# Performance work log

Hardware: AMD Instinct MI355X
Metric: run time of the kernel (lower is better)

Reference implementation:

```python
import jax, jax.numpy as jnp
import numpy as np

T = 4096          # tokens (batch*seq)
D = 768           # moe_intermediate_size (token hidden dim)
I = 2048          # intermediate_size (FFN inner dim)
E = 8             # num_experts


def setup_inputs() -> dict:
    key = jax.random.key(0)
    k_x, k_p, k_g, k_u, k_d = jax.random.split(key, 5)
    hidden_states = jax.random.normal(k_x, (T, D), dtype=jnp.float32)
    position_index = jax.random.randint(k_p, (T,), 0, E, dtype=jnp.int64)
    behavior_index = jnp.zeros((T,), dtype=jnp.int64)  # unused (behavior_injection=False)
    s = 0.02
    # torch Linear weight layout: [out_features, in_features]
    gate_w = jax.random.normal(k_g, (E, I, D), dtype=jnp.float32) * s
    up_w = jax.random.normal(k_u, (E, I, D), dtype=jnp.float32) * s
    down_w = jax.random.normal(k_d, (E, D, I), dtype=jnp.float32) * s
    return {
        "hidden_states": hidden_states,
        "position_index": position_index,
        "behavior_index": behavior_index,
        "gate_w": gate_w,
        "up_w": up_w,
        "down_w": down_w,
    }


def reference(hidden_states, position_index, behavior_index, gate_w, up_w, down_w):
    # Sparse MoE dispatch: each token routed to exactly one expert by position_index.
    # Dropout rate is 0.0 (eval) -> identity. behavior_injection=False -> behavior_index unused.
    num_experts = gate_w.shape[0]
    out = jnp.zeros_like(hidden_states)
    for e in range(num_experts):  # structural loop over fixed expert count
        mask = (position_index == e)[:, None]          # [T, 1]
        g = hidden_states @ gate_w[e].T                 # [T, I]
        u = hidden_states @ up_w[e].T                   # [T, I]
        y = (jax.nn.silu(g) * u) @ down_w[e].T          # [T, D]
        out = out + jnp.where(mask, y, 0.0)             # scatter-combine
    return out
```

## Files before the change

### kernel.cpp

```cpp
#include <hip/hip_runtime.h>
#include <hip/hip_bf16.h>

#define T_TOK 4096
#define DDIM  768
#define IDIM  2048
#define NEXP  8

typedef __attribute__((ext_vector_type(8))) short  bfrag;
typedef __attribute__((ext_vector_type(4))) float  ffrag;

static __device__ __forceinline__ unsigned short f2bf(float f) {
    union { float f; unsigned u; } v; v.f = f;
    unsigned r = v.u + 0x7FFFu + ((v.u >> 16) & 1u);
    return (unsigned short)(r >> 16);
}

static __device__ __forceinline__ unsigned cvt2(float x, float y) {
    return (unsigned)f2bf(x) | ((unsigned)f2bf(y) << 16);
}

__global__ void k_sort(const int* __restrict__ pos, int* __restrict__ ws_i,
                       int* __restrict__ perm) {
    __shared__ int hist[NEXP], cursor[NEXP];
    const int tid = threadIdx.x;
    if (tid < NEXP) hist[tid] = 0;
    __syncthreads();
    for (int i = tid; i < T_TOK; i += 1024)
        atomicAdd(&hist[pos[i]], 1);
    __syncthreads();
    if (tid == 0) {
        int s = 0;
        for (int e = 0; e < NEXP; ++e) {
            cursor[e] = s;
            ws_i[e] = hist[e];
            ws_i[16 + e] = s;
            s += hist[e];
        }
        ws_i[16 + NEXP] = s;
    }
    __syncthreads();
    for (int i = tid; i < T_TOK; i += 1024) {
        int p = atomicAdd(&cursor[pos[i]], 1);
        perm[p] = i;
    }
}

__global__ void k_gather(const float* __restrict__ x, const int* __restrict__ perm,
                         unsigned short* __restrict__ xg) {
    int p = blockIdx.x;
    int tok = perm[p];
    int j = threadIdx.x * 4;
    const float4 v = *reinterpret_cast<const float4*>(x + (size_t)tok * DDIM + j);
    uint2 o;
    o.x = cvt2(v.x, v.y);
    o.y = cvt2(v.z, v.w);
    *reinterpret_cast<uint2*>(xg + (size_t)p * DDIM + j) = o;
}

__launch_bounds__(256, 2)
__global__ void k_gemm1(const unsigned short* __restrict__ xg,
                        const float* __restrict__ gate_w,
                        const float* __restrict__ up_w,
                        unsigned short* __restrict__ hg,
                        const int* __restrict__ ws_i) {
    const int e   = blockIdx.z;
    const int cnt = ws_i[e];
    const int m0  = blockIdx.y * 128;
    if (m0 >= cnt) return;
    const int off = ws_i[16 + e];
    const int n0  = blockIdx.x * 64;

    const int tid  = threadIdx.x;
    const int lane = tid & 63;
    const int wave = tid >> 6;
    const int wm   = wave & 1;
    const int wn   = wave >> 1;

    __shared__ __align__(16) unsigned short lsA[128 * 56];
    __shared__ __align__(16) unsigned short lsG[64 * 56];
    __shared__ __align__(16) unsigned short lsU[64 * 56];

    const float* gate_e = gate_w + (size_t)e * (IDIM * DDIM);
    const float* up_e   = up_w   + (size_t)e * (IDIM * DDIM);

    const int ar = tid >> 2;
    const int aq = tid & 3;
    const int br = tid >> 3;
    const int bq = tid & 7;

    int g0 = off + m0 + ar;      if (g0 > T_TOK - 1) g0 = T_TOK - 1;
    int g1 = off + m0 + ar + 64; if (g1 > T_TOK - 1) g1 = T_TOK - 1;
    const unsigned short* a0p = xg + (size_t)g0 * DDIM + aq * 8;
    const unsigned short* a1p = xg + (size_t)g1 * DDIM + aq * 8;
    const float* gp0 = gate_e + (size_t)(n0 + br)      * DDIM + bq * 4;
    const float* gp1 = gate_e + (size_t)(n0 + br + 32) * DDIM + bq * 4;
    const float* up0 = up_e   + (size_t)(n0 + br)      * DDIM + bq * 4;
    const float* up1 = up_e   + (size_t)(n0 + br + 32) * DDIM + bq * 4;

    uint4  pa0 = *reinterpret_cast<const uint4*>(a0p);
    uint4  pa1 = *reinterpret_cast<const uint4*>(a1p);
    float4 pg0 = *reinterpret_cast<const float4*>(gp0);
    float4 pg1 = *reinterpret_cast<const float4*>(gp1);
    float4 pu0 = *reinterpret_cast<const float4*>(up0);
    float4 pu1 = *reinterpret_cast<const float4*>(up1);

    ffrag accG[4][2], accU[4][2];
    const ffrag fz = {0.f, 0.f, 0.f, 0.f};
    for (int mi = 0; mi < 4; ++mi)
        for (int ni = 0; ni < 2; ++ni) { accG[mi][ni] = fz; accU[mi][ni] = fz; }

    const int koff = (lane >> 4) * 8;
    const int rsel = lane & 15;

    for (int kt = 0; kt < DDIM / 32; ++kt) {
        *reinterpret_cast<uint4*>(&lsA[ar * 56 + aq * 8])        = pa0;
        *reinterpret_cast<uint4*>(&lsA[(ar + 64) * 56 + aq * 8]) = pa1;
        { uint2 o; o.x = cvt2(pg0.x, pg0.y); o.y = cvt2(pg0.z, pg0.w);
          *reinterpret_cast<uint2*>(&lsG[br * 56 + bq * 4]) = o; }
        { uint2 o; o.x = cvt2(pg1.x, pg1.y); o.y = cvt2(pg1.z, pg1.w);
          *reinterpret_cast<uint2*>(&lsG[(br + 32) * 56 + bq * 4]) = o; }
        { uint2 o; o.x = cvt2(pu0.x, pu0.y); o.y = cvt2(pu0.z, pu0.w);
          *reinterpret_cast<uint2*>(&lsU[br * 56 + bq * 4]) = o; }
        { uint2 o; o.x = cvt2(pu1.x, pu1.y); o.y = cvt2(pu1.z, pu1.w);
          *reinterpret_cast<uint2*>(&lsU[(br + 32) * 56 + bq * 4]) = o; }
        __syncthreads();

        if (kt < DDIM / 32 - 1) {
            const int kb = (kt + 1) * 32;
            pa0 = *reinterpret_cast<const uint4*>(a0p + kb);
            pa1 = *reinterpret_cast<const uint4*>(a1p + kb);
            pg0 = *reinterpret_cast<const float4*>(gp0 + kb);
            pg1 = *reinterpret_cast<const float4*>(gp1 + kb);
            pu0 = *reinterpret_cast<const float4*>(up0 + kb);
            pu1 = *reinterpret_cast<const float4*>(up1 + kb);
        }

        bfrag a[4], bg[2], bu[2];
        #pragma unroll
        for (int mi = 0; mi < 4; ++mi)
            a[mi] = *reinterpret_cast<const bfrag*>(&lsA[(wm * 64 + mi * 16 + rsel) * 56 + koff]);
        #pragma unroll
        for (int ni = 0; ni < 2; ++ni) {
            bg[ni] = *reinterpret_cast<const bfrag*>(&lsG[(wn * 32 + ni * 16 + rsel) * 56 + koff]);
            bu[ni] = *reinterpret_cast<const bfrag*>(&lsU[(wn * 32 + ni * 16 + rsel) * 56 + koff]);
        }
        #pragma unroll
        for (int mi = 0; mi < 4; ++mi)
            #pragma unroll
            for (int ni = 0; ni < 2; ++ni) {
                accG[mi][ni] = __builtin_amdgcn_mfma_f32_16x16x32_bf16(a[mi], bg[ni], accG[mi][ni], 0, 0, 0);
                accU[mi][ni] = __builtin_amdgcn_mfma_f32_16x16x32_bf16(a[mi], bu[ni], accU[mi][ni], 0, 0, 0);
            }
        __syncthreads();
    }

    const int colb  = lane & 15;
    const int rquad = (lane >> 4) * 4;
    #pragma unroll
    for (int mi = 0; mi < 4; ++mi)
        #pragma unroll
        for (int ni = 0; ni < 2; ++ni) {
            int n = n0 + wn * 32 + ni * 16 + colb;
            #pragma unroll
            for (int r = 0; r < 4; ++r) {
                int ml = wm * 64 + mi * 16 + rquad + r;
                if (m0 + ml < cnt) {
                    float g = accG[mi][ni][r];
                    float u = accU[mi][ni][r];
                    float h = (g / (1.0f + __expf(-g))) * u;
                    hg[(size_t)(off + m0 + ml) * IDIM + n] = f2bf(h);
                }
            }
        }
}

__launch_bounds__(256, 2)
__global__ void k_gemm2(const unsigned short* __restrict__ hg,
                        const float* __restrict__ down_w,
                        float* __restrict__ out,
                        const int* __restrict__ ws_i,
                        const int* __restrict__ perm) {
    const int e     = blockIdx.z & 7;
    const int split = blockIdx.z >> 3;
    const int cnt = ws_i[e];
    const int m0  = blockIdx.y * 128;
    if (m0 >= cnt) return;
    const int off = ws_i[16 + e];
    const int n0  = blockIdx.x * 64;

    const int tid  = threadIdx.x;
    const int lane = tid & 63;
    const int wave = tid >> 6;
    const int wm   = wave & 1;
    const int wn   = wave >> 1;

    __shared__ __align__(16) unsigned short lsA[128 * 56];
    __shared__ __align__(16) unsigned short lsB[64 * 56];

    const float* down_e = down_w + (size_t)e * (DDIM * IDIM);

    const int ar = tid >> 2;
    const int aq = tid & 3;
    const int br = tid >> 3;
    const int bq = tid & 7;

    int g0 = off + m0 + ar;      if (g0 > T_TOK - 1) g0 = T_TOK - 1;
    int g1 = off + m0 + ar + 64; if (g1 > T_TOK - 1) g1 = T_TOK - 1;
    const unsigned short* a0p = hg + (size_t)g0 * IDIM + split * 512 + aq * 8;
    const unsigned short* a1p = hg + (size_t)g1 * IDIM + split * 512 + aq * 8;
    const float* bp0 = down_e + (size_t)(n0 + br)      * IDIM + split * 512 + bq * 4;
    const float* bp1 = down_e + (size_t)(n0 + br + 32) * IDIM + split * 512 + bq * 4;

    uint4  pa0 = *reinterpret_cast<const uint4*>(a0p);
    uint4  pa1 = *reinterpret_cast<const uint4*>(a1p);
    float4 pb0 = *reinterpret_cast<const float4*>(bp0);
    float4 pb1 = *reinterpret_cast<const float4*>(bp1);

    ffrag acc[4][2];
    const ffrag fz = {0.f, 0.f, 0.f, 0.f};
    for (int mi = 0; mi < 4; ++mi)
        for (int ni = 0; ni < 2; ++ni) acc[mi][ni] = fz;

    const int koff = (lane >> 4) * 8;
    const int rsel = lane & 15;

    for (int kt = 0; kt < 16; ++kt) {
        *reinterpret_cast<uint4*>(&lsA[ar * 56 + aq * 8])        = pa0;
        *reinterpret_cast<uint4*>(&lsA[(ar + 64) * 56 + aq * 8]) = pa1;
        { uint2 o; o.x = cvt2(pb0.x, pb0.y); o.y = cvt2(pb0.z, pb0.w);
          *reinterpret_cast<uint2*>(&lsB[br * 56 + bq * 4]) = o; }
        { uint2 o; o.x = cvt2(pb1.x, pb1.y); o.y = cvt2(pb1.z, pb1.w);
          *reinterpret_cast<uint2*>(&lsB[(br + 32) * 56 + bq * 4]) = o; }
        __syncthreads();

        if (kt < 15) {
            const int kb = (kt + 1) * 32;
            pa0 = *reinterpret_cast<const uint4*>(a0p + kb);
            pa1 = *reinterpret_cast<const uint4*>(a1p + kb);
            pb0 = *reinterpret_cast<const float4*>(bp0 + kb);
            pb1 = *reinterpret_cast<const float4*>(bp1 + kb);
        }

        bfrag a[4], b[2];
        #pragma unroll
        for (int mi = 0; mi < 4; ++mi)
            a[mi] = *reinterpret_cast<const bfrag*>(&lsA[(wm * 64 + mi * 16 + rsel) * 56 + koff]);
        #pragma unroll
        for (int ni = 0; ni < 2; ++ni)
            b[ni] = *reinterpret_cast<const bfrag*>(&lsB[(wn * 32 + ni * 16 + rsel) * 56 + koff]);
        #pragma unroll
        for (int mi = 0; mi < 4; ++mi)
            #pragma unroll
            for (int ni = 0; ni < 2; ++ni)
                acc[mi][ni] = __builtin_amdgcn_mfma_f32_16x16x32_bf16(a[mi], b[ni], acc[mi][ni], 0, 0, 0);
        __syncthreads();
    }

    const int colb  = lane & 15;
    const int rquad = (lane >> 4) * 4;
    #pragma unroll
    for (int mi = 0; mi < 4; ++mi)
        #pragma unroll
        for (int ni = 0; ni < 2; ++ni) {
            int n = n0 + wn * 32 + ni * 16 + colb;
            #pragma unroll
            for (int r = 0; r < 4; ++r) {
                int ml = wm * 64 + mi * 16 + rquad + r;
                if (m0 + ml < cnt) {
                    int tok = perm[off + m0 + ml];
                    unsafeAtomicAdd(&out[(size_t)tok * DDIM + n], acc[mi][ni][r]);
                }
            }
        }
}

extern "C" void kernel_launch(void* const* d_in, const int* in_sizes, int n_in,
                              void* d_out, int out_size, void* d_ws, size_t ws_size,
                              hipStream_t stream) {
    const float* x      = (const float*)d_in[0];
    const int*   pos    = (const int*)d_in[1];
    const float* gate_w = (const float*)d_in[3];
    const float* up_w   = (const float*)d_in[4];
    const float* down_w = (const float*)d_in[5];
    float* out = (float*)d_out;

    char* ws = (char*)d_ws;
    int* ws_i = (int*)ws;
    int* perm = (int*)(ws + 1024);
    unsigned short* xg = (unsigned short*)(ws + 32768);
    unsigned short* hg = (unsigned short*)(ws + (8u << 20));

    (void)hipMemsetAsync(d_out, 0, (size_t)out_size * sizeof(float), stream);
    k_sort<<<dim3(1), dim3(1024), 0, stream>>>(pos, ws_i, perm);
    k_gather<<<dim3(T_TOK), dim3(192), 0, stream>>>(x, perm, xg);

    dim3 g1(IDIM / 64, 32, NEXP);
    k_gemm1<<<g1, dim3(256), 0, stream>>>(xg, gate_w, up_w, hg, ws_i);
    dim3 g2(DDIM / 64, 32, NEXP * 4);
    k_gemm2<<<g2, dim3(256), 0, stream>>>(hg, down_w, out, ws_i, perm);
}
```

Before: 305.0 us.

## Double-buffer LDS in both GEMMs and drop split-K atomics in down projection

Both GEMM kernels now use double-buffered shared memory with a narrower padded row stride, overlapping global loads, LDS stores and MFMA compute with one barrier per stage. The down-projection kernel no longer splits K four ways with atomic adds. It uses 64-row tiles over the full K range and writes outputs directly, which also removes the output memset. The trade-off is fewer blocks and a longer serial K loop per block in gemm2, alongside higher occupancy targets in the launch bounds.

```diff
diff --git a/kernel.cpp b/kernel.cpp
--- a/kernel.cpp
+++ b/kernel.cpp
@@ -5,6 +5,7 @@
 #define DDIM  768
 #define IDIM  2048
 #define NEXP  8
+#define LSTR  40
 
 typedef __attribute__((ext_vector_type(8))) short  bfrag;
 typedef __attribute__((ext_vector_type(4))) float  ffrag;
@@ -18,6 +19,12 @@
 static __device__ __forceinline__ unsigned cvt2(float x, float y) {
     return (unsigned)f2bf(x) | ((unsigned)f2bf(y) << 16);
 }
+
+#define PIPE_BAR() do { \
+    asm volatile("s_waitcnt lgkmcnt(0)" ::: "memory"); \
+    __builtin_amdgcn_s_barrier(); \
+    __builtin_amdgcn_sched_barrier(0); \
+} while (0)
 
 __global__ void k_sort(const int* __restrict__ pos, int* __restrict__ ws_i,
                        int* __restrict__ perm) {
@@ -57,7 +64,7 @@
     *reinterpret_cast<uint2*>(xg + (size_t)p * DDIM + j) = o;
 }
 
-__launch_bounds__(256, 2)
+__launch_bounds__(256, 3)
 __global__ void k_gemm1(const unsigned short* __restrict__ xg,
                         const float* __restrict__ gate_w,
                         const float* __restrict__ up_w,
@@ -76,9 +83,9 @@
     const int wm   = wave & 1;
     const int wn   = wave >> 1;
 
-    __shared__ __align__(16) unsigned short lsA[128 * 56];
-    __shared__ __align__(16) unsigned short lsG[64 * 56];
-    __shared__ __align__(16) unsigned short lsU[64 * 56];
+    __shared__ __align__(16) unsigned short lsA[2][128 * LSTR];
+    __shared__ __align__(16) unsigned short lsG[2][64 * LSTR];
+    __shared__ __align__(16) unsigned short lsU[2][64 * LSTR];
 
     const float* gate_e = gate_w + (size_t)e * (IDIM * DDIM);
     const float* up_e   = up_w   + (size_t)e * (IDIM * DDIM);
@@ -97,13 +104,6 @@
     const float* up0 = up_e   + (size_t)(n0 + br)      * DDIM + bq * 4;
     const float* up1 = up_e   + (size_t)(n0 + br + 32) * DDIM + bq * 4;
 
-    uint4  pa0 = *reinterpret_cast<const uint4*>(a0p);
-    uint4  pa1 = *reinterpret_cast<const uint4*>(a1p);
-    float4 pg0 = *reinterpret_cast<const float4*>(gp0);
-    float4 pg1 = *reinterpret_cast<const float4*>(gp1);
-    float4 pu0 = *reinterpret_cast<const float4*>(up0);
-    float4 pu1 = *reinterpret_cast<const float4*>(up1);
-
     ffrag accG[4][2], accU[4][2];
     const ffrag fz = {0.f, 0.f, 0.f, 0.f};
     for (int mi = 0; mi < 4; ++mi)
@@ -112,47 +112,66 @@
     const int koff = (lane >> 4) * 8;
     const int rsel = lane & 15;
 
-    for (int kt = 0; kt < DDIM / 32; ++kt) {
-        *reinterpret_cast<uint4*>(&lsA[ar * 56 + aq * 8])        = pa0;
-        *reinterpret_cast<uint4*>(&lsA[(ar + 64) * 56 + aq * 8]) = pa1;
-        { uint2 o; o.x = cvt2(pg0.x, pg0.y); o.y = cvt2(pg0.z, pg0.w);
-          *reinterpret_cast<uint2*>(&lsG[br * 56 + bq * 4]) = o; }
-        { uint2 o; o.x = cvt2(pg1.x, pg1.y); o.y = cvt2(pg1.z, pg1.w);
-          *reinterpret_cast<uint2*>(&lsG[(br + 32) * 56 + bq * 4]) = o; }
-        { uint2 o; o.x = cvt2(pu0.x, pu0.y); o.y = cvt2(pu0.z, pu0.w);
-          *reinterpret_cast<uint2*>(&lsU[br * 56 + bq * 4]) = o; }
-        { uint2 o; o.x = cvt2(pu1.x, pu1.y); o.y = cvt2(pu1.z, pu1.w);
-          *reinterpret_cast<uint2*>(&lsU[(br + 32) * 56 + bq * 4]) = o; }
-        __syncthreads();
-
-        if (kt < DDIM / 32 - 1) {
-            const int kb = (kt + 1) * 32;
-            pa0 = *reinterpret_cast<const uint4*>(a0p + kb);
-            pa1 = *reinterpret_cast<const uint4*>(a1p + kb);
-            pg0 = *reinterpret_cast<const float4*>(gp0 + kb);
-            pg1 = *reinterpret_cast<const float4*>(gp1 + kb);
-            pu0 = *reinterpret_cast<const float4*>(up0 + kb);
-            pu1 = *reinterpret_cast<const float4*>(up1 + kb);
-        }
-
-        bfrag a[4], bg[2], bu[2];
-        #pragma unroll
-        for (int mi = 0; mi < 4; ++mi)
-            a[mi] = *reinterpret_cast<const bfrag*>(&lsA[(wm * 64 + mi * 16 + rsel) * 56 + koff]);
-        #pragma unroll
-        for (int ni = 0; ni < 2; ++ni) {
-            bg[ni] = *reinterpret_cast<const bfrag*>(&lsG[(wn * 32 + ni * 16 + rsel) * 56 + koff]);
-            bu[ni] = *reinterpret_cast<const bfrag*>(&lsU[(wn * 32 + ni * 16 + rsel) * 56 + koff]);
-        }
-        #pragma unroll
-        for (int mi = 0; mi < 4; ++mi)
-            #pragma unroll
-            for (int ni = 0; ni < 2; ++ni) {
-                accG[mi][ni] = __builtin_amdgcn_mfma_f32_16x16x32_bf16(a[mi], bg[ni], accG[mi][ni], 0, 0, 0);
-                accU[mi][ni] = __builtin_amdgcn_mfma_f32_16x16x32_bf16(a[mi], bu[ni], accU[mi][ni], 0, 0, 0);
-            }
-        __syncthreads();
+    uint4 Ea0, Ea1; float4 Eg0, Eg1, Eu0, Eu1;
+    uint4 Oa0, Oa1; float4 Og0, Og1, Ou0, Ou1;
+
+#define G1_LOAD(Pa0,Pa1,Pg0,Pg1,Pu0,Pu1, kb) do { \
+    Pa0 = *reinterpret_cast<const uint4*>(a0p + (kb)); \
+    Pa1 = *reinterpret_cast<const uint4*>(a1p + (kb)); \
+    Pg0 = *reinterpret_cast<const float4*>(gp0 + (kb)); \
+    Pg1 = *reinterpret_cast<const float4*>(gp1 + (kb)); \
+    Pu0 = *reinterpret_cast<const float4*>(up0 + (kb)); \
+    Pu1 = *reinterpret_cast<const float4*>(up1 + (kb)); } while (0)
+
+#define G1_STORE(B, Pa0,Pa1,Pg0,Pg1,Pu0,Pu1) do { \
+    *reinterpret_cast<uint4*>(&lsA[B][ar * LSTR + aq * 8])        = Pa0; \
+    *reinterpret_cast<uint4*>(&lsA[B][(ar + 64) * LSTR + aq * 8]) = Pa1; \
+    { uint2 o; o.x = cvt2(Pg0.x, Pg0.y); o.y = cvt2(Pg0.z, Pg0.w); \
+      *reinterpret_cast<uint2*>(&lsG[B][br * LSTR + bq * 4]) = o; } \
+    { uint2 o; o.x = cvt2(Pg1.x, Pg1.y); o.y = cvt2(Pg1.z, Pg1.w); \
+      *reinterpret_cast<uint2*>(&lsG[B][(br + 32) * LSTR + bq * 4]) = o; } \
+    { uint2 o; o.x = cvt2(Pu0.x, Pu0.y); o.y = cvt2(Pu0.z, Pu0.w); \
+      *reinterpret_cast<uint2*>(&lsU[B][br * LSTR + bq * 4]) = o; } \
+    { uint2 o; o.x = cvt2(Pu1.x, Pu1.y); o.y = cvt2(Pu1.z, Pu1.w); \
+      *reinterpret_cast<uint2*>(&lsU[B][(br + 32) * LSTR + bq * 4]) = o; } } while (0)
+
+#define G1_COMPUTE(B) do { \
+    bfrag a[4], bg[2], bu[2]; \
+    _Pragma("unroll") \
+    for (int mi = 0; mi < 4; ++mi) \
+        a[mi] = *reinterpret_cast<const bfrag*>(&lsA[B][(wm * 64 + mi * 16 + rsel) * LSTR + koff]); \
+    _Pragma("unroll") \
+    for (int ni = 0; ni < 2; ++ni) { \
+        bg[ni] = *reinterpret_cast<const bfrag*>(&lsG[B][(wn * 32 + ni * 16 + rsel) * LSTR + koff]); \
+        bu[ni] = *reinterpret_cast<const bfrag*>(&lsU[B][(wn * 32 + ni * 16 + rsel) * LSTR + koff]); \
+    } \
+    _Pragma("unroll") \
+    for (int mi = 0; mi < 4; ++mi) { \
+        _Pragma("unroll") \
+        for (int ni = 0; ni < 2; ++ni) { \
+            accG[mi][ni] = __builtin_amdgcn_mfma_f32_16x16x32_bf16(a[mi], bg[ni], accG[mi][ni], 0, 0, 0); \
+            accU[mi][ni] = __builtin_amdgcn_mfma_f32_16x16x32_bf16(a[mi], bu[ni], accU[mi][ni], 0, 0, 0); \
+        } \
+    } } while (0)
+
+    G1_LOAD(Ea0, Ea1, Eg0, Eg1, Eu0, Eu1, 0);
+    G1_STORE(0, Ea0, Ea1, Eg0, Eg1, Eu0, Eu1);
+    G1_LOAD(Oa0, Oa1, Og0, Og1, Ou0, Ou1, 32);
+    PIPE_BAR();
+
+    for (int kt = 0; kt < 24; kt += 2) {
+        if (kt + 2 < 24) G1_LOAD(Ea0, Ea1, Eg0, Eg1, Eu0, Eu1, kt * 32 + 64);
+        G1_COMPUTE(0);
+        G1_STORE(1, Oa0, Oa1, Og0, Og1, Ou0, Ou1);
+        PIPE_BAR();
+        if (kt + 3 < 24) G1_LOAD(Oa0, Oa1, Og0, Og1, Ou0, Ou1, kt * 32 + 96);
+        G1_COMPUTE(1);
+        if (kt + 2 < 24) G1_STORE(0, Ea0, Ea1, Eg0, Eg1, Eu0, Eu1);
+        PIPE_BAR();
     }
+#undef G1_LOAD
+#undef G1_STORE
+#undef G1_COMPUTE
 
     const int colb  = lane & 15;
     const int rquad = (lane >> 4) * 4;
@@ -174,16 +193,15 @@
         }
 }
 
-__launch_bounds__(256, 2)
+__launch_bounds__(256, 4)
 __global__ void k_gemm2(const unsigned short* __restrict__ hg,
                         const float* __restrict__ down_w,
                         float* __restrict__ out,
                         const int* __restrict__ ws_i,
                         const int* __restrict__ perm) {
-    const int e     = blockIdx.z & 7;
-    const int split = blockIdx.z >> 3;
+    const int e   = blockIdx.z;
     const int cnt = ws_i[e];
-    const int m0  = blockIdx.y * 128;
+    const int m0  = blockIdx.y * 64;
     if (m0 >= cnt) return;
     const int off = ws_i[16 + e];
     const int n0  = blockIdx.x * 64;
@@ -194,8 +212,8 @@
     const int wm   = wave & 1;
     const int wn   = wave >> 1;
 
-    __shared__ __align__(16) unsigned short lsA[128 * 56];
-    __shared__ __align__(16) unsigned short lsB[64 * 56];
+    __shared__ __align__(16) unsigned short lsA[2][64 * LSTR];
+    __shared__ __align__(16) unsigned short lsB[2][64 * LSTR];
 
     const float* down_e = down_w + (size_t)e * (DDIM * IDIM);
 
@@ -204,71 +222,81 @@
     const int br = tid >> 3;
     const int bq = tid & 7;
 
-    int g0 = off + m0 + ar;      if (g0 > T_TOK - 1) g0 = T_TOK - 1;
-    int g1 = off + m0 + ar + 64; if (g1 > T_TOK - 1) g1 = T_TOK - 1;
-    const unsigned short* a0p = hg + (size_t)g0 * IDIM + split * 512 + aq * 8;
-    const unsigned short* a1p = hg + (size_t)g1 * IDIM + split * 512 + aq * 8;
-    const float* bp0 = down_e + (size_t)(n0 + br)      * IDIM + split * 512 + bq * 4;
-    const float* bp1 = down_e + (size_t)(n0 + br + 32) * IDIM + split * 512 + bq * 4;
-
-    uint4  pa0 = *reinterpret_cast<const uint4*>(a0p);
-    uint4  pa1 = *reinterpret_cast<const uint4*>(a1p);
-    float4 pb0 = *reinterpret_cast<const float4*>(bp0);
-    float4 pb1 = *reinterpret_cast<const float4*>(bp1);
-
-    ffrag acc[4][2];
+    int g0 = off + m0 + ar; if (g0 > T_TOK - 1) g0 = T_TOK - 1;
+    const unsigned short* a0p = hg + (size_t)g0 * IDIM + aq * 8;
+    const float* bp0 = down_e + (size_t)(n0 + br)      * IDIM + bq * 4;
+    const float* bp1 = down_e + (size_t)(n0 + br + 32) * IDIM + bq * 4;
+
+    ffrag acc[2][2];
     const ffrag fz = {0.f, 0.f, 0.f, 0.f};
-    for (int mi = 0; mi < 4; ++mi)
+    for (int mi = 0; mi < 2; ++mi)
         for (int ni = 0; ni < 2; ++ni) acc[mi][ni] = fz;
 
     const int koff = (lane >> 4) * 8;
     const int rsel = lane & 15;
 
-    for (int kt = 0; kt < 16; ++kt) {
-        *reinterpret_cast<uint4*>(&lsA[ar * 56 + aq * 8])        = pa0;
-        *reinterpret_cast<uint4*>(&lsA[(ar + 64) * 56 + aq * 8]) = pa1;
-        { uint2 o; o.x = cvt2(pb0.x, pb0.y); o.y = cvt2(pb0.z, pb0.w);
-          *reinterpret_cast<uint2*>(&lsB[br * 56 + bq * 4]) = o; }
-        { uint2 o; o.x = cvt2(pb1.x, pb1.y); o.y = cvt2(pb1.z, pb1.w);
-          *reinterpret_cast<uint2*>(&lsB[(br + 32) * 56 + bq * 4]) = o; }
-        __syncthreads();
-
-        if (kt < 15) {
-            const int kb = (kt + 1) * 32;
-            pa0 = *reinterpret_cast<const uint4*>(a0p + kb);
-            pa1 = *reinterpret_cast<const uint4*>(a1p + kb);
-            pb0 = *reinterpret_cast<const float4*>(bp0 + kb);
-            pb1 = *reinterpret_cast<const float4*>(bp1 + kb);
-        }
-
-        bfrag a[4], b[2];
-        #pragma unroll
-        for (int mi = 0; mi < 4; ++mi)
-            a[mi] = *reinterpret_cast<const bfrag*>(&lsA[(wm * 64 + mi * 16 + rsel) * 56 + koff]);
-        #pragma unroll
-        for (int ni = 0; ni < 2; ++ni)
-            b[ni] = *reinterpret_cast<const bfrag*>(&lsB[(wn * 32 + ni * 16 + rsel) * 56 + koff]);
-        #pragma unroll
-        for (int mi = 0; mi < 4; ++mi)
-            #pragma unroll
-            for (int ni = 0; ni < 2; ++ni)
-                acc[mi][ni] = __builtin_amdgcn_mfma_f32_16x16x32_bf16(a[mi], b[ni], acc[mi][ni], 0, 0, 0);
-        __syncthreads();
+    uint4 Ea; float4 Eb0, Eb1;
+    uint4 Oa; float4 Ob0, Ob1;
+
+#define G2_LOAD(Pa,Pb0,Pb1, kb) do { \
+    Pa  = *reinterpret_cast<const uint4*>(a0p + (kb)); \
+    Pb0 = *reinterpret_cast<const float4*>(bp0 + (kb)); \
+    Pb1 = *reinterpret_cast<const float4*>(bp1 + (kb)); } while (0)
+
+#define G2_STORE(B, Pa,Pb0,Pb1) do { \
+    *reinterpret_cast<uint4*>(&lsA[B][ar * LSTR + aq * 8]) = Pa; \
+    { uint2 o; o.x = cvt2(Pb0.x, Pb0.y); o.y = cvt2(Pb0.z, Pb0.w); \
+      *reinterpret_cast<uint2*>(&lsB[B][br * LSTR + bq * 4]) = o; } \
+    { uint2 o; o.x = cvt2(Pb1.x, Pb1.y); o.y = cvt2(Pb1.z, Pb1.w); \
+      *reinterpret_cast<uint2*>(&lsB[B][(br + 32) * LSTR + bq * 4]) = o; } } while (0)
+
+#define G2_COMPUTE(B) do { \
+    bfrag a[2], b[2]; \
+    _Pragma("unroll") \
+    for (int mi = 0; mi < 2; ++mi) \
+        a[mi] = *reinterpret_cast<const bfrag*>(&lsA[B][(wm * 32 + mi * 16 + rsel) * LSTR + koff]); \
+    _Pragma("unroll") \
+    for (int ni = 0; ni < 2; ++ni) \
+        b[ni] = *reinterpret_cast<const bfrag*>(&lsB[B][(wn * 32 + ni * 16 + rsel) * LSTR + koff]); \
+    _Pragma("unroll") \
+    for (int mi = 0; mi < 2; ++mi) { \
+        _Pragma("unroll") \
+        for (int ni = 0; ni < 2; ++ni) \
+            acc[mi][ni] = __builtin_amdgcn_mfma_f32_16x16x32_bf16(a[mi], b[ni], acc[mi][ni], 0, 0, 0); \
+    } } while (0)
+
+    G2_LOAD(Ea, Eb0, Eb1, 0);
+    G2_STORE(0, Ea, Eb0, Eb1);
+    G2_LOAD(Oa, Ob0, Ob1, 32);
+    PIPE_BAR();
+
+    for (int kt = 0; kt < 64; kt += 2) {
+        if (kt + 2 < 64) G2_LOAD(Ea, Eb0, Eb1, kt * 32 + 64);
+        G2_COMPUTE(0);
+        G2_STORE(1, Oa, Ob0, Ob1);
+        PIPE_BAR();
+        if (kt + 3 < 64) G2_LOAD(Oa, Ob0, Ob1, kt * 32 + 96);
+        G2_COMPUTE(1);
+        if (kt + 2 < 64) G2_STORE(0, Ea, Eb0, Eb1);
+        PIPE_BAR();
     }
+#undef G2_LOAD
+#undef G2_STORE
+#undef G2_COMPUTE
 
     const int colb  = lane & 15;
     const int rquad = (lane >> 4) * 4;
     #pragma unroll
-    for (int mi = 0; mi < 4; ++mi)
+    for (int mi = 0; mi < 2; ++mi)
         #pragma unroll
         for (int ni = 0; ni < 2; ++ni) {
             int n = n0 + wn * 32 + ni * 16 + colb;
             #pragma unroll
             for (int r = 0; r < 4; ++r) {
-                int ml = wm * 64 + mi * 16 + rquad + r;
+                int ml = wm * 32 + mi * 16 + rquad + r;
                 if (m0 + ml < cnt) {
                     int tok = perm[off + m0 + ml];
-                    unsafeAtomicAdd(&out[(size_t)tok * DDIM + n], acc[mi][ni][r]);
+                    out[(size_t)tok * DDIM + n] = acc[mi][ni][r];
                 }
             }
         }
@@ -290,12 +318,11 @@
     unsigned short* xg = (unsigned short*)(ws + 32768);
     unsigned short* hg = (unsigned short*)(ws + (8u << 20));
 
-    (void)hipMemsetAsync(d_out, 0, (size_t)out_size * sizeof(float), stream);
     k_sort<<<dim3(1), dim3(1024), 0, stream>>>(pos, ws_i, perm);
     k_gather<<<dim3(T_TOK), dim3(192), 0, stream>>>(x, perm, xg);
 
-    dim3 g1(IDIM / 64, 32, NEXP);
+    dim3 g1(IDIM / 64, T_TOK / 128, NEXP);
     k_gemm1<<<g1, dim3(256), 0, stream>>>(xg, gate_w, up_w, hg, ws_i);
-    dim3 g2(DDIM / 64, 32, NEXP * 4);
+    dim3 g2(DDIM / 64, T_TOK / 64, NEXP);
     k_gemm2<<<g2, dim3(256), 0, stream>>>(hg, down_w, out, ws_i, perm);
 }
```

Measured after the change: 427.2 us. 40.1% more time.
